# Optimization experiments

Hardware: AMD Instinct MI355X
Metric: run time of the kernel (lower is better)

## Reference

```python
import jax, jax.numpy as jnp
import numpy as np

NC = 80          # num classes
REG_MAX = 16     # DFL bins
STRIDES = (8, 16, 32)
FEAT_HW = ((80, 80), (40, 40), (20, 20))
MAX_DET = 100
CONF_THRES = 0.25
IOU_THRES = 0.45
PRE_TOPK = 1000  # pre-NMS candidate count (EfficientNMS-style preselection)


def setup_inputs() -> dict:
    key = jax.random.key(0)
    k1, k2, k3 = jax.random.split(key, 3)
    B = 32
    no = 4 * REG_MAX + NC  # 144
    return {
        "p3": jax.random.normal(k1, (B, no, 80, 80), dtype=jnp.float32),
        "p4": jax.random.normal(k2, (B, no, 40, 40), dtype=jnp.float32),
        "p5": jax.random.normal(k3, (B, no, 20, 20), dtype=jnp.float32),
    }


def _make_anchors():
    # grid_cell_offset = 0.5, matching ultralytics make_anchors
    pts, strs = [], []
    for (h, w), s in zip(FEAT_HW, STRIDES):
        sx = jnp.arange(w, dtype=jnp.float32) + 0.5
        sy = jnp.arange(h, dtype=jnp.float32) + 0.5
        yy, xx = jnp.meshgrid(sy, sx, indexing="ij")
        pts.append(jnp.stack([xx.ravel(), yy.ravel()], axis=-1))  # [h*w, 2]
        strs.append(jnp.full((h * w, 1), float(s), dtype=jnp.float32))
    return jnp.concatenate(pts, 0), jnp.concatenate(strs, 0)  # [A,2], [A,1]


def _pairwise_iou(b):
    # b: [K, 4] xyxy
    area = (b[:, 2] - b[:, 0]) * (b[:, 3] - b[:, 1])
    lt = jnp.maximum(b[:, None, :2], b[None, :, :2])
    rb = jnp.minimum(b[:, None, 2:], b[None, :, 2:])
    wh = jnp.clip(rb - lt, 0.0)
    inter = wh[..., 0] * wh[..., 1]
    return inter / (area[:, None] + area[None, :] - inter + 1e-7)


def _nms_single(bxyxy, conf):
    # Greedy class-agnostic NMS over PRE_TOPK score-sorted boxes.
    K = bxyxy.shape[0]
    iou = _pairwise_iou(bxyxy)  # [K, K]
    idx = jnp.arange(K)

    def step(suppressed, xs):
        i, row = xs
        keep = jnp.logical_and(jnp.logical_not(suppressed[i]), conf[i] > 0.0)
        suppressed = jnp.logical_or(suppressed, keep & (row > IOU_THRES) & (idx > i))
        return suppressed, keep

    _, keeps = jax.lax.scan(step, jnp.zeros(K, dtype=bool), (idx, iou))
    return keeps  # [K] bool


def reference(p3, p4, p5):
    feats = [p3, p4, p5]
    B = p3.shape[0]
    no = 4 * REG_MAX + NC
    # concat across scales: [B, no, A]
    x_cat = jnp.concatenate([f.reshape(B, no, -1) for f in feats], axis=2)
    box, cls = x_cat[:, : 4 * REG_MAX], x_cat[:, 4 * REG_MAX:]

    anchors, strd = _make_anchors()  # [A,2], [A,1]
    A = box.shape[-1]

    # DFL: softmax over reg_max bins, expectation with arange weights
    prob = jax.nn.softmax(box.reshape(B, 4, REG_MAX, A), axis=2)
    dist = jnp.einsum("bkra,r->bka", prob, jnp.arange(REG_MAX, dtype=jnp.float32))

    # dist2bbox (xywh) then scale by stride
    anc = anchors.T  # [2, A]
    lt, rb = dist[:, :2], dist[:, 2:]
    x1y1 = anc - lt
    x2y2 = anc + rb
    dbox = jnp.concatenate([(x1y1 + x2y2) * 0.5, x2y2 - x1y1], axis=1) * strd.T  # [B,4,A]

    boxes = dbox.transpose(0, 2, 1)                       # [B, A, 4] xywh
    scores = jax.nn.sigmoid(cls).transpose(0, 2, 1)       # [B, A, NC] (score_activation=1)

    # class-agnostic: best class per box
    conf = scores.max(-1)                                 # [B, A]
    cls_id = jnp.argmax(scores, -1)                       # [B, A]
    conf_m = jnp.where(conf > CONF_THRES, conf, -1.0)

    topv, topi = jax.lax.top_k(conf_m, PRE_TOPK)          # [B, K]
    bsel = jnp.take_along_axis(boxes, topi[..., None], axis=1)  # [B, K, 4]
    cx, cy, w, h = bsel[..., 0], bsel[..., 1], bsel[..., 2], bsel[..., 3]
    bxyxy = jnp.stack([cx - w * 0.5, cy - h * 0.5, cx + w * 0.5, cy + h * 0.5], -1)

    keeps = jax.vmap(_nms_single)(bxyxy, topv)            # [B, K]
    kept_scores = jnp.where(keeps, topv, -1.0)
    dv, di = jax.lax.top_k(kept_scores, MAX_DET)          # [B, MAX_DET]
    valid = dv > 0.0

    det_scores = jnp.where(valid, dv, 0.0)
    det_boxes = jnp.take_along_axis(bxyxy, di[..., None], axis=1) * valid[..., None]
    sel_cls = jnp.take_along_axis(jnp.take_along_axis(cls_id, topi, 1), di, 1)
    det_classes = jnp.where(valid, sel_cls, 0).astype(jnp.int32)
    num_dets = valid.sum(-1, keepdims=True).astype(jnp.int32)
    return num_dets, det_boxes, det_scores, det_classes
```

## Files before the change

kernel.cpp:

```cpp
#include <hip/hip_runtime.h>
#include <math.h>

#define NCLS 80
#define NA 8400
#define NB 32
#define NO 144
#define PRE_TOPK 1000
#define MAX_DET 100

__device__ __forceinline__ float dfl16(const float* v) {
    float mm = v[0];
    #pragma unroll
    for (int r = 1; r < 16; ++r) mm = fmaxf(mm, v[r]);
    float sum = 0.f, d = 0.f;
    #pragma unroll
    for (int r = 0; r < 16; ++r) {
        float e = __expf(v[r] - mm);
        sum += e;
        d += e * (float)r;
    }
    return d * (1.0f / sum);
}

__device__ __forceinline__ void cls20(const float* v, int chbase, float& best, int& bid) {
    float m = v[0]; int ii = 0;
    #pragma unroll
    for (int c = 1; c < 20; ++c) if (v[c] > m) { m = v[c]; ii = c; }
    if (m > best) { best = m; bid = chbase + ii; }
}

template<int HW, int WDIM, int S>
__device__ __forceinline__ void decode_store(
    const float* __restrict__ src, int g, int aoff,
    float* __restrict__ conf, int* __restrict__ clsid, float* __restrict__ box)
{
    int b = g / HW;
    int pos = g - b * HW;
    float ax = (float)(pos % WDIM) + 0.5f;
    float ay = (float)(pos / WDIM) + 0.5f;
    const float* base = src + (size_t)b * (NO * HW) + pos;

    float g0[16], g1[16], g2[16], g3[16];
    float c0[20], c1[20], c2[20], c3[20];

    #pragma unroll
    for (int r = 0; r < 16; ++r) g0[r] = base[(size_t)r * HW];
    #pragma unroll
    for (int r = 0; r < 16; ++r) g1[r] = base[(size_t)(16 + r) * HW];
    #pragma unroll
    for (int r = 0; r < 16; ++r) g2[r] = base[(size_t)(32 + r) * HW];
    #pragma unroll
    for (int r = 0; r < 16; ++r) g3[r] = base[(size_t)(48 + r) * HW];
    float d0 = dfl16(g0);
    float d1 = dfl16(g1);
    #pragma unroll
    for (int c = 0; c < 20; ++c) c0[c] = base[(size_t)(64 + c) * HW];
    #pragma unroll
    for (int c = 0; c < 20; ++c) c1[c] = base[(size_t)(84 + c) * HW];
    float d2 = dfl16(g2);
    float d3 = dfl16(g3);
    #pragma unroll
    for (int c = 0; c < 20; ++c) c2[c] = base[(size_t)(104 + c) * HW];
    #pragma unroll
    for (int c = 0; c < 20; ++c) c3[c] = base[(size_t)(124 + c) * HW];
    float best = -INFINITY; int bid = 0;
    cls20(c0, 0, best, bid);
    cls20(c1, 20, best, bid);
    cls20(c2, 40, best, bid);
    cls20(c3, 60, best, bid);

    float conf_v = 1.0f / (1.0f + __expf(-best));

    float x1 = ax - d0, y1 = ay - d1;
    float x2 = ax + d2, y2 = ay + d3;
    float cx = ((x1 + x2) * 0.5f) * (float)S;
    float cy = ((y1 + y2) * 0.5f) * (float)S;
    float w  = (x2 - x1) * (float)S;
    float h  = (y2 - y1) * (float)S;

    size_t gid = (size_t)b * NA + aoff + pos;
    conf[gid]  = conf_v;
    clsid[gid] = bid;
    *(float4*)(box + gid * 4) = make_float4(cx, cy, w, h);
}

__global__ __launch_bounds__(256, 4) void k_decode(
    const float* __restrict__ p3, const float* __restrict__ p4, const float* __restrict__ p5,
    float* __restrict__ conf, int* __restrict__ clsid, float* __restrict__ box)
{
    int blk = blockIdx.x;
    int t = threadIdx.x;
    if (blk < 800) {
        int g = blk * 256 + t;
        decode_store<6400, 80, 8>(p3, g, 0, conf, clsid, box);
    } else if (blk < 1000) {
        int g = (blk - 800) * 256 + t;
        decode_store<1600, 40, 16>(p4, g, 6400, conf, clsid, box);
    } else {
        int g = (blk - 1000) * 256 + t;
        decode_store<400, 20, 32>(p5, g, 8000, conf, clsid, box);
    }
}

__device__ __forceinline__ uint32_t ord_bits(float f) {
    uint32_t u = __float_as_uint(f);
    return (u & 0x80000000u) ? ~u : (u | 0x80000000u);
}

__global__ __launch_bounds__(1024) void k_select(
    const float* __restrict__ conf, const float* __restrict__ box, const int* __restrict__ clsid,
    float* __restrict__ topv, float* __restrict__ bxyxy, int* __restrict__ topcls)
{
    int b = blockIdx.x;
    int t = threadIdx.x;
    int lane = t & 63;

    __shared__ uint32_t ob[NA];
    __shared__ uint32_t hist[256];
    __shared__ uint64_t sbuf[1024];
    __shared__ uint64_t s_prefix;
    __shared__ int s_k;
    __shared__ int s_cnt;

    const float* cf = conf + (size_t)b * NA;
    for (int i = t; i < NA; i += 1024) {
        float c = cf[i];
        float cm = (c > 0.25f) ? c : -1.0f;
        ob[i] = ord_bits(cm);
    }
    if (t == 0) { s_prefix = 0; s_k = PRE_TOPK; s_cnt = 0; }
    sbuf[t] = 0;
    __syncthreads();

    for (int pass = 0; pass < 8; ++pass) {
        int shift = 56 - 8 * pass;
        if (t < 256) hist[t] = 0;
        __syncthreads();
        uint64_t prefix = s_prefix;
        int k = s_k;
        for (int i = t; i < NA; i += 1024) {
            uint64_t key = ((uint64_t)ob[i] << 32) | (uint64_t)(0xFFFFFFFFu - (uint32_t)i);
            bool match = (pass == 0) || (((key ^ prefix) >> (64 - 8 * pass)) == 0);
            uint32_t d = (uint32_t)(key >> shift) & 255u;
            if (match) {
                uint64_t m = __ballot(1);
                #pragma unroll
                for (int bb = 0; bb < 8; ++bb) {
                    uint64_t bal = __ballot((d >> bb) & 1u);
                    m &= ((d >> bb) & 1u) ? bal : ~bal;
                }
                if ((m & ((1ull << lane) - 1ull)) == 0ull)
                    atomicAdd(&hist[d], (uint32_t)__popcll(m));
            }
        }
        __syncthreads();
        if (t < 64) {
            uint32_t h0 = hist[4 * t + 0], h1 = hist[4 * t + 1];
            uint32_t h2 = hist[4 * t + 2], h3 = hist[4 * t + 3];
            uint32_t part = h0 + h1 + h2 + h3;
            uint32_t s = part;
            #pragma unroll
            for (int off = 1; off < 64; off <<= 1) {
                uint32_t v = __shfl_down(s, off);
                if (t + off < 64) s += v;
            }
            uint32_t cb3 = s - part;
            uint32_t cb2 = cb3 + h3;
            uint32_t cb1 = cb2 + h2;
            uint32_t cb0 = cb1 + h1;
            uint32_t ku = (uint32_t)k;
            if (cb3 < ku && ku <= cb3 + h3) { s_k = k - (int)cb3; s_prefix = prefix | ((uint64_t)(uint32_t)(4 * t + 3) << shift); }
            if (cb2 < ku && ku <= cb2 + h2) { s_k = k - (int)cb2; s_prefix = prefix | ((uint64_t)(uint32_t)(4 * t + 2) << shift); }
            if (cb1 < ku && ku <= cb1 + h1) { s_k = k - (int)cb1; s_prefix = prefix | ((uint64_t)(uint32_t)(4 * t + 1) << shift); }
            if (cb0 < ku && ku <= cb0 + h0) { s_k = k - (int)cb0; s_prefix = prefix | ((uint64_t)(uint32_t)(4 * t + 0) << shift); }
        }
        __syncthreads();
    }

    uint64_t kstar = s_prefix;
    for (int i = t; i < NA; i += 1024) {
        uint64_t key = ((uint64_t)ob[i] << 32) | (uint64_t)(0xFFFFFFFFu - (uint32_t)i);
        if (key >= kstar) {
            int p = atomicAdd(&s_cnt, 1);
            if (p < 1024) sbuf[p] = key;
        }
    }
    __syncthreads();

    uint64_t v = sbuf[t];
    for (int k = 2; k <= 1024; k <<= 1) {
        for (int j = k >> 1; j > 0; j >>= 1) {
            uint64_t o;
            if (j >= 64) {
                sbuf[t] = v;
                __syncthreads();
                o = sbuf[t ^ j];
                __syncthreads();
            } else {
                o = __shfl_xor((unsigned long long)v, j);
            }
            bool desc  = ((t & k) == 0);
            bool lower = ((t & j) == 0);
            v = (desc == lower) ? (v > o ? v : o) : (v < o ? v : o);
        }
    }

    if (t < PRE_TOPK) {
        uint64_t key = v;
        uint32_t u = (uint32_t)(key >> 32);
        uint32_t fb = (u & 0x80000000u) ? (u ^ 0x80000000u) : ~u;
        float val = __uint_as_float(fb);
        int idx = (int)(0xFFFFFFFFu - (uint32_t)(key & 0xFFFFFFFFull));
        size_t g = (size_t)b * NA + idx;
        float4 bx = *(const float4*)(box + g * 4);
        float cx = bx.x, cy = bx.y, w = bx.z, h = bx.w;
        size_t o = (size_t)b * PRE_TOPK + t;
        topv[o] = val;
        *(float4*)(bxyxy + o * 4) = make_float4(cx - w * 0.5f, cy - h * 0.5f,
                                                cx + w * 0.5f, cy + h * 0.5f);
        topcls[o] = clsid[g];
    }
}

__device__ __forceinline__ int bslot(int j) { return j + (j >> 6); }

__global__ __launch_bounds__(256) void k_iou(
    const float* __restrict__ bxyxy, unsigned long long* __restrict__ mask)
{
    __shared__ float4 boxes[PRE_TOPK + 16];
    int b = blockIdx.y;
    int t = threadIdx.x;
    const float4* bp = (const float4*)(bxyxy + (size_t)b * PRE_TOPK * 4);
    for (int i = t; i < PRE_TOPK; i += 256) boxes[bslot(i)] = bp[i];
    __syncthreads();

    int r_local = t >> 4, w = t & 15;
    int row = blockIdx.x * 16 + r_local;
    if (row >= PRE_TOPK) return;

    float4 bi = boxes[bslot(row)];
    float area_i = (bi.z - bi.x) * (bi.w - bi.y);
    unsigned long long bits = 0;
    int j0 = w * 64;
    #pragma unroll 4
    for (int jj = 0; jj < 64; ++jj) {
        int j = j0 + jj;
        if (j >= PRE_TOPK) break;
        if (j <= row) continue;
        float4 bj = boxes[bslot(j)];
        float lx = fmaxf(bi.x, bj.x), ly = fmaxf(bi.y, bj.y);
        float rx = fminf(bi.z, bj.z), ry = fminf(bi.w, bj.w);
        float iw = fmaxf(rx - lx, 0.f), ih = fmaxf(ry - ly, 0.f);
        float inter = iw * ih;
        float area_j = (bj.z - bj.x) * (bj.w - bj.y);
        float iou = inter / (area_i + area_j - inter + 1e-7f);
        if (iou > 0.45f) bits |= (1ull << jj);
    }
    mask[((size_t)b * PRE_TOPK + row) * 16 + w] = bits;
}

__global__ __launch_bounds__(1024) void k_nms(
    const unsigned long long* __restrict__ mask, const float* __restrict__ topv,
    const float* __restrict__ bxyxy, const int* __restrict__ topcls,
    float* __restrict__ out)
{
    int b = blockIdx.x;
    int t = threadIdx.x;

    __shared__ __align__(16) unsigned long long smask[PRE_TOPK * 16];
    __shared__ float sv[PRE_TOPK];
    __shared__ unsigned long long s_valid[16];
    __shared__ int kept[MAX_DET];
    __shared__ int s_cnt;

    for (int i = t; i < PRE_TOPK; i += 1024) sv[i] = topv[(size_t)b * PRE_TOPK + i];
    {
        const ulonglong2* src = (const ulonglong2*)(mask + (size_t)b * PRE_TOPK * 16);
        ulonglong2* dst = (ulonglong2*)smask;
        for (int i = t; i < PRE_TOPK * 8; i += 1024) dst[i] = src[i];
    }
    __syncthreads();

    {
        bool pred = (t < PRE_TOPK) && (sv[t] > 0.0f);
        unsigned long long bal = __ballot(pred);
        if ((t & 63) == 0) s_valid[t >> 6] = bal;
    }
    __syncthreads();

    if (t < 64) {
        int w = t;
        unsigned long long supp = 0;
        unsigned long long valid = (w < 16) ? s_valid[w] : 0ull;
        int base = w * 64;
        int cur = -1;
        int cnt = 0;
        while (cnt < MAX_DET) {
            unsigned long long gt;
            if (cur < base)            gt = ~0ull;
            else if (cur - base >= 63) gt = 0ull;
            else                       gt = (~0ull) << (cur - base + 1);
            unsigned long long cand = valid & ~supp & gt;
            int idx = cand ? (base + __builtin_ctzll(cand)) : 0x7FFFFFFF;
            #pragma unroll
            for (int off = 8; off >= 1; off >>= 1) {
                int o = __shfl_xor(idx, off);
                idx = (o < idx) ? o : idx;
            }
            int nxt = __shfl(idx, 0);
            if (nxt == 0x7FFFFFFF) break;
            if (t == 0) kept[cnt] = nxt;
            ++cnt;
            if (w < 16) supp |= smask[nxt * 16 + w];
            cur = nxt;
        }
        if (t == 0) s_cnt = cnt;
    }
    __syncthreads();

    int cnt = s_cnt; if (cnt > MAX_DET) cnt = MAX_DET;
    if (t == 0) out[b] = (float)cnt;
    if (t < MAX_DET) {
        bool valid = t < cnt;
        float bx0 = 0.f, bx1 = 0.f, bx2 = 0.f, bx3 = 0.f, sc = 0.f, cl = 0.f;
        if (valid) {
            int p = kept[t];
            size_t o = (size_t)b * PRE_TOPK + p;
            float4 bb = *(const float4*)(bxyxy + o * 4);
            bx0 = bb.x; bx1 = bb.y; bx2 = bb.z; bx3 = bb.w;
            sc = sv[p];
            cl = (float)topcls[o];
        }
        size_t db = 32 + ((size_t)b * MAX_DET + t) * 4;
        out[db + 0] = bx0; out[db + 1] = bx1; out[db + 2] = bx2; out[db + 3] = bx3;
        out[32 + 12800 + (size_t)b * MAX_DET + t] = sc;
        out[32 + 16000 + (size_t)b * MAX_DET + t] = cl;
    }
}

extern "C" void kernel_launch(void* const* d_in, const int* in_sizes, int n_in,
                              void* d_out, int out_size, void* d_ws, size_t ws_size,
                              hipStream_t stream)
{
    const float* p3 = (const float*)d_in[0];
    const float* p4 = (const float*)d_in[1];
    const float* p5 = (const float*)d_in[2];
    float* out = (float*)d_out;

    char* ws = (char*)d_ws;
    size_t off_mask = 0;
    size_t off_conf = off_mask + (size_t)NB * PRE_TOPK * 16 * 8;
    size_t off_cls  = off_conf + (size_t)NB * NA * 4;
    size_t off_box  = off_cls  + (size_t)NB * NA * 4;
    size_t off_topv = off_box  + (size_t)NB * NA * 4 * 4;
    size_t off_topc = off_topv + (size_t)NB * PRE_TOPK * 4;
    size_t off_bx   = off_topc + (size_t)NB * PRE_TOPK * 4;

    unsigned long long* mask = (unsigned long long*)(ws + off_mask);
    float* conf   = (float*)(ws + off_conf);
    int*   clsid  = (int*)(ws + off_cls);
    float* box    = (float*)(ws + off_box);
    float* topv   = (float*)(ws + off_topv);
    int*   topcls = (int*)(ws + off_topc);
    float* bxyxy  = (float*)(ws + off_bx);

    k_decode<<<1050, 256, 0, stream>>>(p3, p4, p5, conf, clsid, box);
    k_select<<<NB, 1024, 0, stream>>>(conf, box, clsid, topv, bxyxy, topcls);
    k_iou<<<dim3((PRE_TOPK + 15) / 16, NB), 256, 0, stream>>>(bxyxy, mask);
    k_nms<<<NB, 1024, 0, stream>>>(mask, topv, bxyxy, topcls, out);
}
```

Before: 154.7 us.

## Split decode of each anchor across four threads with shared-memory reduction

The decode kernel now assigns 64 anchors per block and gives each anchor four threads, each handling one DFL side and one 20-class slice. Partial DFL distances and class maxima go through shared memory, and the first wavefront combines them and writes conf, class id and box. This is meant to cut per-thread register pressure and raise memory-level parallelism on the bandwidth-bound read of the 144-channel inputs. The cost is a block barrier, shared-memory traffic, idle threads during the final stage, and partially filled blocks at the tail of each scale.

Measured after the change: 142.1 us. -8.1%, faster.

```diff
diff --git a/kernel.cpp b/kernel.cpp
--- a/kernel.cpp
+++ b/kernel.cpp
@@ -8,7 +8,28 @@
 #define PRE_TOPK 1000
 #define MAX_DET 100
 
-__device__ __forceinline__ float dfl16(const float* v) {
+template<int HW, int WDIM, int S>
+__device__ __forceinline__ void decode_blk(
+    const float* __restrict__ src, int b, int a0, int aoff,
+    float* __restrict__ conf, int* __restrict__ clsid, float* __restrict__ box)
+{
+    __shared__ float s_dfl[64 * 5];
+    __shared__ float s_mx[64 * 5];
+    __shared__ int   s_id[64 * 5];
+
+    int t  = threadIdx.x;
+    int p  = t >> 6;
+    int al = t & 63;
+    int pos = a0 + al;
+    int posc = pos < HW ? pos : HW - 1;
+    const float* base = src + (size_t)b * (NO * HW) + posc;
+
+    float v[16], c[20];
+    #pragma unroll
+    for (int r = 0; r < 16; ++r) v[r] = base[(size_t)(p * 16 + r) * HW];
+    #pragma unroll
+    for (int cc = 0; cc < 20; ++cc) c[cc] = base[(size_t)(64 + p * 20 + cc) * HW];
+
     float mm = v[0];
     #pragma unroll
     for (int r = 1; r < 16; ++r) mm = fmaxf(mm, v[r]);
@@ -19,87 +40,53 @@
         sum += e;
         d += e * (float)r;
     }
-    return d * (1.0f / sum);
-}
-
-__device__ __forceinline__ void cls20(const float* v, int chbase, float& best, int& bid) {
-    float m = v[0]; int ii = 0;
-    #pragma unroll
-    for (int c = 1; c < 20; ++c) if (v[c] > m) { m = v[c]; ii = c; }
-    if (m > best) { best = m; bid = chbase + ii; }
-}
-
-template<int HW, int WDIM, int S>
-__device__ __forceinline__ void decode_store(
-    const float* __restrict__ src, int g, int aoff,
-    float* __restrict__ conf, int* __restrict__ clsid, float* __restrict__ box)
-{
-    int b = g / HW;
-    int pos = g - b * HW;
-    float ax = (float)(pos % WDIM) + 0.5f;
-    float ay = (float)(pos / WDIM) + 0.5f;
-    const float* base = src + (size_t)b * (NO * HW) + pos;
-
-    float g0[16], g1[16], g2[16], g3[16];
-    float c0[20], c1[20], c2[20], c3[20];
-
-    #pragma unroll
-    for (int r = 0; r < 16; ++r) g0[r] = base[(size_t)r * HW];
-    #pragma unroll
-    for (int r = 0; r < 16; ++r) g1[r] = base[(size_t)(16 + r) * HW];
-    #pragma unroll
-    for (int r = 0; r < 16; ++r) g2[r] = base[(size_t)(32 + r) * HW];
-    #pragma unroll
-    for (int r = 0; r < 16; ++r) g3[r] = base[(size_t)(48 + r) * HW];
-    float d0 = dfl16(g0);
-    float d1 = dfl16(g1);
-    #pragma unroll
-    for (int c = 0; c < 20; ++c) c0[c] = base[(size_t)(64 + c) * HW];
-    #pragma unroll
-    for (int c = 0; c < 20; ++c) c1[c] = base[(size_t)(84 + c) * HW];
-    float d2 = dfl16(g2);
-    float d3 = dfl16(g3);
-    #pragma unroll
-    for (int c = 0; c < 20; ++c) c2[c] = base[(size_t)(104 + c) * HW];
-    #pragma unroll
-    for (int c = 0; c < 20; ++c) c3[c] = base[(size_t)(124 + c) * HW];
-    float best = -INFINITY; int bid = 0;
-    cls20(c0, 0, best, bid);
-    cls20(c1, 20, best, bid);
-    cls20(c2, 40, best, bid);
-    cls20(c3, 60, best, bid);
-
-    float conf_v = 1.0f / (1.0f + __expf(-best));
-
-    float x1 = ax - d0, y1 = ay - d1;
-    float x2 = ax + d2, y2 = ay + d3;
-    float cx = ((x1 + x2) * 0.5f) * (float)S;
-    float cy = ((y1 + y2) * 0.5f) * (float)S;
-    float w  = (x2 - x1) * (float)S;
-    float h  = (y2 - y1) * (float)S;
-
-    size_t gid = (size_t)b * NA + aoff + pos;
-    conf[gid]  = conf_v;
-    clsid[gid] = bid;
-    *(float4*)(box + gid * 4) = make_float4(cx, cy, w, h);
-}
-
-__global__ __launch_bounds__(256, 4) void k_decode(
+    d *= 1.0f / sum;
+
+    float m = c[0]; int ii = 0;
+    #pragma unroll
+    for (int cc = 1; cc < 20; ++cc) if (c[cc] > m) { m = c[cc]; ii = cc; }
+
+    s_dfl[al * 5 + p] = d;
+    s_mx[al * 5 + p]  = m;
+    s_id[al * 5 + p]  = p * 20 + ii;
+    __syncthreads();
+
+    if (t < 64 && a0 + t < HW) {
+        int pos2 = a0 + t;
+        float d0 = s_dfl[t * 5 + 0], d1 = s_dfl[t * 5 + 1];
+        float d2 = s_dfl[t * 5 + 2], d3 = s_dfl[t * 5 + 3];
+        float bm = s_mx[t * 5 + 0]; int bid = s_id[t * 5 + 0];
+        float m1 = s_mx[t * 5 + 1]; if (m1 > bm) { bm = m1; bid = s_id[t * 5 + 1]; }
+        float m2 = s_mx[t * 5 + 2]; if (m2 > bm) { bm = m2; bid = s_id[t * 5 + 2]; }
+        float m3 = s_mx[t * 5 + 3]; if (m3 > bm) { bm = m3; bid = s_id[t * 5 + 3]; }
+        float conf_v = 1.0f / (1.0f + __expf(-bm));
+
+        float ax = (float)(pos2 % WDIM) + 0.5f;
+        float ay = (float)(pos2 / WDIM) + 0.5f;
+        float x1 = ax - d0, y1 = ay - d1;
+        float x2 = ax + d2, y2 = ay + d3;
+        float cx = ((x1 + x2) * 0.5f) * (float)S;
+        float cy = ((y1 + y2) * 0.5f) * (float)S;
+        float w  = (x2 - x1) * (float)S;
+        float h  = (y2 - y1) * (float)S;
+
+        size_t gid = (size_t)b * NA + aoff + pos2;
+        conf[gid]  = conf_v;
+        clsid[gid] = bid;
+        *(float4*)(box + gid * 4) = make_float4(cx, cy, w, h);
+    }
+}
+
+__global__ __launch_bounds__(256) void k_decode(
     const float* __restrict__ p3, const float* __restrict__ p4, const float* __restrict__ p5,
     float* __restrict__ conf, int* __restrict__ clsid, float* __restrict__ box)
 {
     int blk = blockIdx.x;
-    int t = threadIdx.x;
-    if (blk < 800) {
-        int g = blk * 256 + t;
-        decode_store<6400, 80, 8>(p3, g, 0, conf, clsid, box);
-    } else if (blk < 1000) {
-        int g = (blk - 800) * 256 + t;
-        decode_store<1600, 40, 16>(p4, g, 6400, conf, clsid, box);
-    } else {
-        int g = (blk - 1000) * 256 + t;
-        decode_store<400, 20, 32>(p5, g, 8000, conf, clsid, box);
-    }
+    int b = blk / 132;
+    int r = blk - b * 132;
+    if (r < 100)       decode_blk<6400, 80, 8>(p3, b, r * 64, 0, conf, clsid, box);
+    else if (r < 125)  decode_blk<1600, 40, 16>(p4, b, (r - 100) * 64, 6400, conf, clsid, box);
+    else               decode_blk<400, 20, 32>(p5, b, (r - 125) * 64, 8000, conf, clsid, box);
 }
 
 __device__ __forceinline__ uint32_t ord_bits(float f) {
@@ -364,7 +351,7 @@
     int*   topcls = (int*)(ws + off_topc);
     float* bxyxy  = (float*)(ws + off_bx);
 
-    k_decode<<<1050, 256, 0, stream>>>(p3, p4, p5, conf, clsid, box);
+    k_decode<<<NB * 132, 256, 0, stream>>>(p3, p4, p5, conf, clsid, box);
     k_select<<<NB, 1024, 0, stream>>>(conf, box, clsid, topv, bxyxy, topcls);
     k_iou<<<dim3((PRE_TOPK + 15) / 16, NB), 256, 0, stream>>>(bxyxy, mask);
     k_nms<<<NB, 1024, 0, stream>>>(mask, topv, bxyxy, topcls, out);
```
